# Performance work log

Measured on AMD Instinct MI355X. Metric: run time of the kernel, lower is better.

The kernel has to match this reference:

```python
import jax, jax.numpy as jnp
import numpy as np

H = 128  # hidden size
I = 19   # input size


def _uniform(key, shape, bound):
    return jax.random.uniform(key, shape, dtype=jnp.float32, minval=-bound, maxval=bound)


def setup_inputs() -> dict:
    key = jax.random.key(0)
    ks = jax.random.split(key, 9)
    bound = 1.0 / np.sqrt(H)  # torch nn.RNN init: U(-1/sqrt(H), 1/sqrt(H))
    x = jax.random.normal(ks[0], (256, 1024, I), dtype=jnp.float32)
    return {
        "x": x,
        "W_ih0": _uniform(ks[1], (H, I), bound),
        "W_hh0": _uniform(ks[2], (H, H), bound),
        "b_ih0": _uniform(ks[3], (H,), bound),
        "b_hh0": _uniform(ks[4], (H,), bound),
        "W_ih1": _uniform(ks[5], (H, H), bound),
        "W_hh1": _uniform(ks[6], (H, H), bound),
        "b_ih1": _uniform(ks[7], (H,), bound),
        "b_hh1": _uniform(ks[8], (H,), bound),
    }


def _rnn_layer(inp, W_ih, W_hh, b_ih, b_hh):
    # inp: [B, T, F]. Precompute input projection for all timesteps (one big GEMM),
    # then scan only the recurrent part: h_t = tanh(pre_t + h_{t-1} @ W_hh^T).
    pre = jnp.einsum('btf,hf->bth', inp, W_ih) + b_ih + b_hh  # [B, T, H]
    h0 = jnp.zeros((inp.shape[0], H), dtype=inp.dtype)

    def step(h, p_t):
        h = jnp.tanh(p_t + h @ W_hh.T)
        return h, h

    _, ys = jax.lax.scan(step, h0, jnp.swapaxes(pre, 0, 1))  # ys: [T, B, H]
    return jnp.swapaxes(ys, 0, 1)  # [B, T, H]


def reference(x, W_ih0, W_hh0, b_ih0, b_hh0, W_ih1, W_hh1, b_ih1, b_hh1):
    out1 = _rnn_layer(x, W_ih0, W_hh0, b_ih0, b_hh0)
    out2 = _rnn_layer(out1, W_ih1, W_hh1, b_ih1, b_hh1)
    return out2
```

## Files before the change

kernel.cpp:

```cpp
#include <hip/hip_runtime.h>
#include <math.h>

#define BATCH 256
#define T 1024
#define IN 19
#define H 128

__device__ __forceinline__ float fast_tanh(float x) {
    float ax = fabsf(x);
    float e  = __expf(2.0f * ax);
    float r  = 1.0f - 2.0f / (e + 1.0f);
    return copysignf(r, x);
}

template <int CTRL>
__device__ __forceinline__ float dppf(float v) {
    return __int_as_float(__builtin_amdgcn_update_dpp(
        0, __float_as_int(v), CTRL, 0xF, 0xF, true));
}
#define XOR1 0xB1
#define XOR2 0x4E
#define XOR8 0x128

__device__ __forceinline__ void sync_fast() {
    asm volatile("s_waitcnt lgkmcnt(0)" ::: "memory");
    __builtin_amdgcn_s_barrier();
    asm volatile("" ::: "memory");
}

__device__ __forceinline__ int uoff(int u) { return (u >> 4) * 20 + (u & 15); }

__global__ __launch_bounds__(512, 2)
void fused_rnn(const float* __restrict__ x,
               const float* __restrict__ Wih0,
               const float* __restrict__ Whh0,
               const float* __restrict__ bih0,
               const float* __restrict__ bhh0,
               const float* __restrict__ Wih1,
               const float* __restrict__ Whh1,
               const float* __restrict__ bih1,
               const float* __restrict__ bhh1,
               float* __restrict__ out) {
    const int b   = blockIdx.x;
    const int tid = threadIdx.x;

    __shared__ __align__(16) float h0ring[4][160];
    __shared__ __align__(16) float h1ring[4][160];
    __shared__ __align__(16) float Bring[4][H];
    __shared__ __align__(16) float projring[4][H];
    __shared__ __align__(16) float xbuf[2][8 * 20];

    if (tid < 128) {
        __builtin_amdgcn_s_setprio(1);
        const bool b0 = tid & 1, b1 = tid & 2, b2 = tid & 8;
        const int s    = (tid & 3) | ((tid & 8) >> 1);
        const int G    = (tid >> 4) * 2 + ((tid >> 2) & 1);
        const int ub   = G * 8;
        const int ufin = ub + (b0 ? 4 : 0) + (b1 ? 2 : 0) + (b2 ? 1 : 0);

        float wA[8][16];
#pragma unroll
        for (int u = 0; u < 8; ++u) {
            const float* wr = Whh0 + (size_t)(ub + u) * H + s * 16;
#pragma unroll
            for (int c = 0; c < 16; c += 4) {
                float4 v = *(const float4*)&wr[c];
                wA[u][c] = v.x; wA[u][c+1] = v.y; wA[u][c+2] = v.z; wA[u][c+3] = v.w;
            }
        }
        {
            const float* wr = Wih0 + ufin * IN;
            const float* xr = x + (size_t)b * T * IN;
            float acc = bih0[ufin] + bhh0[ufin];
#pragma unroll
            for (int f = 0; f < IN; ++f) acc = fmaf(xr[f], wr[f], acc);
            projring[0][ufin] = acc;
        }
        h0ring[3][uoff(ufin)] = 0.0f;
        sync_fast();

        const int so = s * 20;
        const int wo = uoff(ufin);
        for (int ko = 0; ko < T; ko += 8) {
#pragma unroll
            for (int j = 0; j < 8; ++j) {
                const float* hp = &h0ring[(j + 3) & 3][so];
                float pcur = projring[j & 3][ufin];
                float d0=0,d1=0,d2=0,d3=0,d4=0,d5=0,d6=0,d7=0;
#pragma unroll
                for (int c = 0; c < 16; c += 4) {
                    float4 hv = *(const float4*)&hp[c];
                    d0 = fmaf(wA[0][c],hv.x,d0); d0 = fmaf(wA[0][c+1],hv.y,d0); d0 = fmaf(wA[0][c+2],hv.z,d0); d0 = fmaf(wA[0][c+3],hv.w,d0);
                    d1 = fmaf(wA[1][c],hv.x,d1); d1 = fmaf(wA[1][c+1],hv.y,d1); d1 = fmaf(wA[1][c+2],hv.z,d1); d1 = fmaf(wA[1][c+3],hv.w,d1);
                    d2 = fmaf(wA[2][c],hv.x,d2); d2 = fmaf(wA[2][c+1],hv.y,d2); d2 = fmaf(wA[2][c+2],hv.z,d2); d2 = fmaf(wA[2][c+3],hv.w,d2);
                    d3 = fmaf(wA[3][c],hv.x,d3); d3 = fmaf(wA[3][c+1],hv.y,d3); d3 = fmaf(wA[3][c+2],hv.z,d3); d3 = fmaf(wA[3][c+3],hv.w,d3);
                    d4 = fmaf(wA[4][c],hv.x,d4); d4 = fmaf(wA[4][c+1],hv.y,d4); d4 = fmaf(wA[4][c+2],hv.z,d4); d4 = fmaf(wA[4][c+3],hv.w,d4);
                    d5 = fmaf(wA[5][c],hv.x,d5); d5 = fmaf(wA[5][c+1],hv.y,d5); d5 = fmaf(wA[5][c+2],hv.z,d5); d5 = fmaf(wA[5][c+3],hv.w,d5);
                    d6 = fmaf(wA[6][c],hv.x,d6); d6 = fmaf(wA[6][c+1],hv.y,d6); d6 = fmaf(wA[6][c+2],hv.z,d6); d6 = fmaf(wA[6][c+3],hv.w,d6);
                    d7 = fmaf(wA[7][c],hv.x,d7); d7 = fmaf(wA[7][c+1],hv.y,d7); d7 = fmaf(wA[7][c+2],hv.z,d7); d7 = fmaf(wA[7][c+3],hv.w,d7);
                }
                float e0 = (b0 ? d4 : d0) + dppf<XOR1>(b0 ? d0 : d4);
                float e1 = (b0 ? d5 : d1) + dppf<XOR1>(b0 ? d1 : d5);
                float e2 = (b0 ? d6 : d2) + dppf<XOR1>(b0 ? d2 : d6);
                float e3 = (b0 ? d7 : d3) + dppf<XOR1>(b0 ? d3 : d7);
                float g0 = (b1 ? e2 : e0) + dppf<XOR2>(b1 ? e0 : e2);
                float g1 = (b1 ? e3 : e1) + dppf<XOR2>(b1 ? e1 : e3);
                float f  = (b2 ? g1 : g0) + dppf<XOR8>(b2 ? g0 : g1);
                h0ring[j & 3][wo] = fast_tanh(pcur + f);
                sync_fast();
            }
        }
        sync_fast();
        sync_fast();
    } else if (tid < 384) {
        const int p  = tid - 128;
        const bool b0 = p & 1, b1 = p & 2;
        const int s    = (p & 3) | ((p & 8) >> 1);
        const int Gp   = (p >> 4) * 2 + ((p >> 2) & 1);
        const int ub   = Gp * 4;
        const int ufin = ub + (b0 ? 2 : 0) + (b1 ? 1 : 0);

        float wP[4][16];
#pragma unroll
        for (int u = 0; u < 4; ++u) {
            const float* wr = Wih1 + (size_t)(ub + u) * H + s * 16;
#pragma unroll
            for (int c = 0; c < 16; c += 4) {
                float4 v = *(const float4*)&wr[c];
                wP[u][c] = v.x; wP[u][c+1] = v.y; wP[u][c+2] = v.z; wP[u][c+3] = v.w;
            }
        }
        const float biasP = bih1[ufin] + bhh1[ufin];

        const bool hasProj = (p >= 128);
        const int pu = p - 128;
        float wIP[20];
        float biasPr = 0.0f;
        const float* xsrc = x + (size_t)b * T * IN + IN;
        const int idx0  = pu;
        const int idx1  = pu + 128;
        const bool v1   = hasProj && (pu < 24);
        const int slot0 = hasProj ? ((idx0 / IN) * 20 + idx0 % IN) : 0;
        const int slot1 = hasProj ? ((idx1 / IN) * 20 + idx1 % IN) : 0;
        const int XMAX  = (T - 1) * IN - 1;
        float xr0 = 0.0f, xr1 = 0.0f;

        if (hasProj) {
            const float* wr = Wih0 + (size_t)pu * IN;
#pragma unroll
            for (int f = 0; f < IN; ++f) wIP[f] = wr[f];
            wIP[19] = 0.0f;
            biasPr = bih0[pu] + bhh0[pu];
            if (pu < 8) { xbuf[0][pu * 20 + 19] = 0.0f; xbuf[1][pu * 20 + 19] = 0.0f; }
            xbuf[0][slot0] = xsrc[idx0];
            if (v1) xbuf[0][slot1] = xsrc[idx1];
            xr0 = xsrc[152 + idx0];
            if (v1) xr1 = xsrc[152 + idx1];
        }
        sync_fast();

        const int so = s * 20;
        for (int ko = 0; ko < T; ko += 8) {
            const int cb = (ko >> 3) & 1;
#pragma unroll
            for (int j = 0; j < 8; ++j) {
                const float* hp = &h0ring[(j + 3) & 3][so];
                float d0=0,d1=0,d2=0,d3=0;
#pragma unroll
                for (int c = 0; c < 16; c += 4) {
                    float4 hv = *(const float4*)&hp[c];
                    d0 = fmaf(wP[0][c],hv.x,d0); d0 = fmaf(wP[0][c+1],hv.y,d0); d0 = fmaf(wP[0][c+2],hv.z,d0); d0 = fmaf(wP[0][c+3],hv.w,d0);
                    d1 = fmaf(wP[1][c],hv.x,d1); d1 = fmaf(wP[1][c+1],hv.y,d1); d1 = fmaf(wP[1][c+2],hv.z,d1); d1 = fmaf(wP[1][c+3],hv.w,d1);
                    d2 = fmaf(wP[2][c],hv.x,d2); d2 = fmaf(wP[2][c+1],hv.y,d2); d2 = fmaf(wP[2][c+2],hv.z,d2); d2 = fmaf(wP[2][c+3],hv.w,d2);
                    d3 = fmaf(wP[3][c],hv.x,d3); d3 = fmaf(wP[3][c+1],hv.y,d3); d3 = fmaf(wP[3][c+2],hv.z,d3); d3 = fmaf(wP[3][c+3],hv.w,d3);
                }
                float e0 = (b0 ? d2 : d0) + dppf<XOR1>(b0 ? d0 : d2);
                float e1 = (b0 ? d3 : d1) + dppf<XOR1>(b0 ? d1 : d3);
                float g  = (b1 ? e1 : e0) + dppf<XOR2>(b1 ? e0 : e1);
                g += dppf<XOR8>(g);
                if (!(p & 8)) Bring[(j + 3) & 3][ufin] = g + biasP;
                if (hasProj) {
                    const float* xp = &xbuf[cb][j * 20];
                    float4 xv0 = *(const float4*)&xp[0];
                    float4 xv1 = *(const float4*)&xp[4];
                    float4 xv2 = *(const float4*)&xp[8];
                    float4 xv3 = *(const float4*)&xp[12];
                    float4 xv4 = *(const float4*)&xp[16];
                    float p0 = biasPr, p1 = 0.0f;
                    p0 = fmaf(xv0.x, wIP[0],  p0); p1 = fmaf(xv0.y, wIP[1],  p1);
                    p0 = fmaf(xv0.z, wIP[2],  p0); p1 = fmaf(xv0.w, wIP[3],  p1);
                    p0 = fmaf(xv1.x, wIP[4],  p0); p1 = fmaf(xv1.y, wIP[5],  p1);
                    p0 = fmaf(xv1.z, wIP[6],  p0); p1 = fmaf(xv1.w, wIP[7],  p1);
                    p0 = fmaf(xv2.x, wIP[8],  p0); p1 = fmaf(xv2.y, wIP[9],  p1);
                    p0 = fmaf(xv2.z, wIP[10], p0); p1 = fmaf(xv2.w, wIP[11], p1);
                    p0 = fmaf(xv3.x, wIP[12], p0); p1 = fmaf(xv3.y, wIP[13], p1);
                    p0 = fmaf(xv3.z, wIP[14], p0); p1 = fmaf(xv3.w, wIP[15], p1);
                    p0 = fmaf(xv4.x, wIP[16], p0); p1 = fmaf(xv4.y, wIP[17], p1);
                    p0 = fmaf(xv4.z, wIP[18], p0); p1 = fmaf(xv4.w, wIP[19], p1);
                    projring[(j + 1) & 3][pu] = p0 + p1;
                    if (j == 7) {
                        float* xd = xbuf[cb ^ 1];
                        xd[slot0] = xr0;
                        if (v1) xd[slot1] = xr1;
                        const int c2 = (ko >> 3) + 2;
                        int o0 = 152 * c2 + idx0; o0 = o0 > XMAX ? XMAX : o0;
                        int o1 = 152 * c2 + idx1; o1 = o1 > XMAX ? XMAX : o1;
                        xr0 = xsrc[o0];
                        if (v1) xr1 = xsrc[o1];
                    }
                }
                sync_fast();
            }
        }
        {
            const float* hp = &h0ring[3][so];
            float d0=0,d1=0,d2=0,d3=0;
#pragma unroll
            for (int c = 0; c < 16; c += 4) {
                float4 hv = *(const float4*)&hp[c];
                d0 = fmaf(wP[0][c],hv.x,d0); d0 = fmaf(wP[0][c+1],hv.y,d0); d0 = fmaf(wP[0][c+2],hv.z,d0); d0 = fmaf(wP[0][c+3],hv.w,d0);
                d1 = fmaf(wP[1][c],hv.x,d1); d1 = fmaf(wP[1][c+1],hv.y,d1); d1 = fmaf(wP[1][c+2],hv.z,d1); d1 = fmaf(wP[1][c+3],hv.w,d1);
                d2 = fmaf(wP[2][c],hv.x,d2); d2 = fmaf(wP[2][c+1],hv.y,d2); d2 = fmaf(wP[2][c+2],hv.z,d2); d2 = fmaf(wP[2][c+3],hv.w,d2);
                d3 = fmaf(wP[3][c],hv.x,d3); d3 = fmaf(wP[3][c+1],hv.y,d3); d3 = fmaf(wP[3][c+2],hv.z,d3); d3 = fmaf(wP[3][c+3],hv.w,d3);
            }
            float e0 = (b0 ? d2 : d0) + dppf<XOR1>(b0 ? d0 : d2);
            float e1 = (b0 ? d3 : d1) + dppf<XOR1>(b0 ? d1 : d3);
            float g  = (b1 ? e1 : e0) + dppf<XOR2>(b1 ? e0 : e1);
            g += dppf<XOR8>(g);
            if (!(p & 8)) Bring[3][ufin] = g + biasP;
        }
        sync_fast();
        sync_fast();
    } else {
        __builtin_amdgcn_s_setprio(1);
        const int w  = tid - 384;
        const bool b0 = w & 1, b1 = w & 2, b2 = w & 8;
        const int s    = (w & 3) | ((w & 8) >> 1);
        const int G    = (w >> 4) * 2 + ((w >> 2) & 1);
        const int ub   = G * 8;
        const int ufin = ub + (b0 ? 4 : 0) + (b1 ? 2 : 0) + (b2 ? 1 : 0);

        float wA[8][16];
#pragma unroll
        for (int u = 0; u < 8; ++u) {
            const float* wr = Whh1 + (size_t)(ub + u) * H + s * 16;
#pragma unroll
            for (int c = 0; c < 16; c += 4) {
                float4 v = *(const float4*)&wr[c];
                wA[u][c] = v.x; wA[u][c+1] = v.y; wA[u][c+2] = v.z; wA[u][c+3] = v.w;
            }
        }
        float* orow = out + (size_t)b * T * H + ufin;
        float sbuf[8];

        h1ring[3][uoff(ufin)] = 0.0f;
        sync_fast();
        sync_fast();
        sync_fast();

        const int so = s * 20;
        const int wo = uoff(ufin);
        for (int ko = 2; ko < 1026; ko += 8) {
#pragma unroll
            for (int j = 0; j < 8; ++j) {
                const float* hp = &h1ring[(j + 3) & 3][so];
                float Bg = Bring[j & 3][ufin];
                float d0=0,d1=0,d2=0,d3=0,d4=0,d5=0,d6=0,d7=0;
#pragma unroll
                for (int c = 0; c < 16; c += 4) {
                    float4 hv = *(const float4*)&hp[c];
                    d0 = fmaf(wA[0][c],hv.x,d0); d0 = fmaf(wA[0][c+1],hv.y,d0); d0 = fmaf(wA[0][c+2],hv.z,d0); d0 = fmaf(wA[0][c+3],hv.w,d0);
                    d1 = fmaf(wA[1][c],hv.x,d1); d1 = fmaf(wA[1][c+1],hv.y,d1); d1 = fmaf(wA[1][c+2],hv.z,d1); d1 = fmaf(wA[1][c+3],hv.w,d1);
                    d2 = fmaf(wA[2][c],hv.x,d2); d2 = fmaf(wA[2][c+1],hv.y,d2); d2 = fmaf(wA[2][c+2],hv.z,d2); d2 = fmaf(wA[2][c+3],hv.w,d2);
                    d3 = fmaf(wA[3][c],hv.x,d3); d3 = fmaf(wA[3][c+1],hv.y,d3); d3 = fmaf(wA[3][c+2],hv.z,d3); d3 = fmaf(wA[3][c+3],hv.w,d3);
                    d4 = fmaf(wA[4][c],hv.x,d4); d4 = fmaf(wA[4][c+1],hv.y,d4); d4 = fmaf(wA[4][c+2],hv.z,d4); d4 = fmaf(wA[4][c+3],hv.w,d4);
                    d5 = fmaf(wA[5][c],hv.x,d5); d5 = fmaf(wA[5][c+1],hv.y,d5); d5 = fmaf(wA[5][c+2],hv.z,d5); d5 = fmaf(wA[5][c+3],hv.w,d5);
                    d6 = fmaf(wA[6][c],hv.x,d6); d6 = fmaf(wA[6][c+1],hv.y,d6); d6 = fmaf(wA[6][c+2],hv.z,d6); d6 = fmaf(wA[6][c+3],hv.w,d6);
                    d7 = fmaf(wA[7][c],hv.x,d7); d7 = fmaf(wA[7][c+1],hv.y,d7); d7 = fmaf(wA[7][c+2],hv.z,d7); d7 = fmaf(wA[7][c+3],hv.w,d7);
                }
                float e0 = (b0 ? d4 : d0) + dppf<XOR1>(b0 ? d0 : d4);
                float e1 = (b0 ? d5 : d1) + dppf<XOR1>(b0 ? d1 : d5);
                float e2 = (b0 ? d6 : d2) + dppf<XOR1>(b0 ? d2 : d6);
                float e3 = (b0 ? d7 : d3) + dppf<XOR1>(b0 ? d3 : d7);
                float g0 = (b1 ? e2 : e0) + dppf<XOR2>(b1 ? e0 : e2);
                float g1 = (b1 ? e3 : e1) + dppf<XOR2>(b1 ? e1 : e3);
                float f  = (b2 ? g1 : g0) + dppf<XOR8>(b2 ? g0 : g1);
                float h1v = fast_tanh(Bg + f);
                h1ring[j & 3][wo] = h1v;
                sbuf[j] = h1v;
                if (j == 7) {
                    const int t0 = ko - 2;
#pragma unroll
                    for (int i = 0; i < 8; ++i)
                        orow[(size_t)(t0 + i) * H] = sbuf[i];
                }
                sync_fast();
            }
        }
    }
}

extern "C" void kernel_launch(void* const* d_in, const int* in_sizes, int n_in,
                              void* d_out, int out_size, void* d_ws, size_t ws_size,
                              hipStream_t stream) {
    const float* x     = (const float*)d_in[0];
    const float* W_ih0 = (const float*)d_in[1];
    const float* W_hh0 = (const float*)d_in[2];
    const float* b_ih0 = (const float*)d_in[3];
    const float* b_hh0 = (const float*)d_in[4];
    const float* W_ih1 = (const float*)d_in[5];
    const float* W_hh1 = (const float*)d_in[6];
    const float* b_ih1 = (const float*)d_in[7];
    const float* b_hh1 = (const float*)d_in[8];

    float* out = (float*)d_out;

    fused_rnn<<<BATCH, 512, 0, stream>>>(x, W_ih0, W_hh0, b_ih0, b_hh0,
                                         W_ih1, W_hh1, b_ih1, b_hh1, out);
}
```

Baseline: 608.7 us.

## Deepen middle-stage pipeline so layer-1 input projection lags one extra step

The middle warp group, which computes W_ih1·h0 for layer 1, now loads h0 into alternating register buffers and computes from the buffer loaded in the previous step. This decouples the shared-memory load from the FMA chain inside each barrier interval. The pipeline gains one more stage: every role adds an extra barrier, and the layer-1 recurrence loop shifts by one step. The aim is to hide LDS latency on the critical path of each step, at the cost of one extra step of pipeline fill and more registers.

```diff
diff --git a/kernel.cpp b/kernel.cpp
--- a/kernel.cpp
+++ b/kernel.cpp
@@ -112,6 +112,7 @@
         }
         sync_fast();
         sync_fast();
+        sync_fast();
     } else if (tid < 384) {
         const int p  = tid - 128;
         const bool b0 = p & 1, b1 = p & 2;
@@ -157,30 +158,75 @@
             xr0 = xsrc[152 + idx0];
             if (v1) xr1 = xsrc[152 + idx1];
         }
-        sync_fast();
+
+        float4 z4 = {0.0f, 0.0f, 0.0f, 0.0f};
+        float4 hA0 = z4, hA1 = z4, hA2 = z4, hA3 = z4;
+        float4 hB0 = z4, hB1 = z4, hB2 = z4, hB3 = z4;
+
+        sync_fast();
+
+#define P_BCOMP(c0, c1, c2v, c3v, BSLOT)                                              \
+        {                                                                             \
+            float d0=0,d1=0,d2=0,d3=0;                                                \
+            d0 = fmaf(wP[0][0],  c0.x, d0); d0 = fmaf(wP[0][1],  c0.y, d0);           \
+            d0 = fmaf(wP[0][2],  c0.z, d0); d0 = fmaf(wP[0][3],  c0.w, d0);           \
+            d1 = fmaf(wP[1][0],  c0.x, d1); d1 = fmaf(wP[1][1],  c0.y, d1);           \
+            d1 = fmaf(wP[1][2],  c0.z, d1); d1 = fmaf(wP[1][3],  c0.w, d1);           \
+            d2 = fmaf(wP[2][0],  c0.x, d2); d2 = fmaf(wP[2][1],  c0.y, d2);           \
+            d2 = fmaf(wP[2][2],  c0.z, d2); d2 = fmaf(wP[2][3],  c0.w, d2);           \
+            d3 = fmaf(wP[3][0],  c0.x, d3); d3 = fmaf(wP[3][1],  c0.y, d3);           \
+            d3 = fmaf(wP[3][2],  c0.z, d3); d3 = fmaf(wP[3][3],  c0.w, d3);           \
+            d0 = fmaf(wP[0][4],  c1.x, d0); d0 = fmaf(wP[0][5],  c1.y, d0);           \
+            d0 = fmaf(wP[0][6],  c1.z, d0); d0 = fmaf(wP[0][7],  c1.w, d0);           \
+            d1 = fmaf(wP[1][4],  c1.x, d1); d1 = fmaf(wP[1][5],  c1.y, d1);           \
+            d1 = fmaf(wP[1][6],  c1.z, d1); d1 = fmaf(wP[1][7],  c1.w, d1);           \
+            d2 = fmaf(wP[2][4],  c1.x, d2); d2 = fmaf(wP[2][5],  c1.y, d2);           \
+            d2 = fmaf(wP[2][6],  c1.z, d2); d2 = fmaf(wP[2][7],  c1.w, d2);           \
+            d3 = fmaf(wP[3][4],  c1.x, d3); d3 = fmaf(wP[3][5],  c1.y, d3);           \
+            d3 = fmaf(wP[3][6],  c1.z, d3); d3 = fmaf(wP[3][7],  c1.w, d3);           \
+            d0 = fmaf(wP[0][8],  c2v.x, d0); d0 = fmaf(wP[0][9],  c2v.y, d0);         \
+            d0 = fmaf(wP[0][10], c2v.z, d0); d0 = fmaf(wP[0][11], c2v.w, d0);         \
+            d1 = fmaf(wP[1][8],  c2v.x, d1); d1 = fmaf(wP[1][9],  c2v.y, d1);         \
+            d1 = fmaf(wP[1][10], c2v.z, d1); d1 = fmaf(wP[1][11], c2v.w, d1);         \
+            d2 = fmaf(wP[2][8],  c2v.x, d2); d2 = fmaf(wP[2][9],  c2v.y, d2);         \
+            d2 = fmaf(wP[2][10], c2v.z, d2); d2 = fmaf(wP[2][11], c2v.w, d2);         \
+            d3 = fmaf(wP[3][8],  c2v.x, d3); d3 = fmaf(wP[3][9],  c2v.y, d3);         \
+            d3 = fmaf(wP[3][10], c2v.z, d3); d3 = fmaf(wP[3][11], c2v.w, d3);         \
+            d0 = fmaf(wP[0][12], c3v.x, d0); d0 = fmaf(wP[0][13], c3v.y, d0);         \
+            d0 = fmaf(wP[0][14], c3v.z, d0); d0 = fmaf(wP[0][15], c3v.w, d0);         \
+            d1 = fmaf(wP[1][12], c3v.x, d1); d1 = fmaf(wP[1][13], c3v.y, d1);         \
+            d1 = fmaf(wP[1][14], c3v.z, d1); d1 = fmaf(wP[1][15], c3v.w, d1);         \
+            d2 = fmaf(wP[2][12], c3v.x, d2); d2 = fmaf(wP[2][13], c3v.y, d2);         \
+            d2 = fmaf(wP[2][14], c3v.z, d2); d2 = fmaf(wP[2][15], c3v.w, d2);         \
+            d3 = fmaf(wP[3][12], c3v.x, d3); d3 = fmaf(wP[3][13], c3v.y, d3);         \
+            d3 = fmaf(wP[3][14], c3v.z, d3); d3 = fmaf(wP[3][15], c3v.w, d3);         \
+            float e0 = (b0 ? d2 : d0) + dppf<XOR1>(b0 ? d0 : d2);                     \
+            float e1 = (b0 ? d3 : d1) + dppf<XOR1>(b0 ? d1 : d3);                     \
+            float g  = (b1 ? e1 : e0) + dppf<XOR2>(b1 ? e0 : e1);                     \
+            g += dppf<XOR8>(g);                                                       \
+            if (!(p & 8)) Bring[BSLOT][ufin] = g + biasP;                             \
+        }
 
         const int so = s * 20;
         for (int ko = 0; ko < T; ko += 8) {
             const int cb = (ko >> 3) & 1;
 #pragma unroll
-            for (int j = 0; j < 8; ++j) {
-                const float* hp = &h0ring[(j + 3) & 3][so];
-                float d0=0,d1=0,d2=0,d3=0;
-#pragma unroll
-                for (int c = 0; c < 16; c += 4) {
-                    float4 hv = *(const float4*)&hp[c];
-                    d0 = fmaf(wP[0][c],hv.x,d0); d0 = fmaf(wP[0][c+1],hv.y,d0); d0 = fmaf(wP[0][c+2],hv.z,d0); d0 = fmaf(wP[0][c+3],hv.w,d0);
-                    d1 = fmaf(wP[1][c],hv.x,d1); d1 = fmaf(wP[1][c+1],hv.y,d1); d1 = fmaf(wP[1][c+2],hv.z,d1); d1 = fmaf(wP[1][c+3],hv.w,d1);
-                    d2 = fmaf(wP[2][c],hv.x,d2); d2 = fmaf(wP[2][c+1],hv.y,d2); d2 = fmaf(wP[2][c+2],hv.z,d2); d2 = fmaf(wP[2][c+3],hv.w,d2);
-                    d3 = fmaf(wP[3][c],hv.x,d3); d3 = fmaf(wP[3][c+1],hv.y,d3); d3 = fmaf(wP[3][c+2],hv.z,d3); d3 = fmaf(wP[3][c+3],hv.w,d3);
-                }
-                float e0 = (b0 ? d2 : d0) + dppf<XOR1>(b0 ? d0 : d2);
-                float e1 = (b0 ? d3 : d1) + dppf<XOR1>(b0 ? d1 : d3);
-                float g  = (b1 ? e1 : e0) + dppf<XOR2>(b1 ? e0 : e1);
-                g += dppf<XOR8>(g);
-                if (!(p & 8)) Bring[(j + 3) & 3][ufin] = g + biasP;
+            for (int jj = 0; jj < 8; ++jj) {
+                const float* hp = &h0ring[(jj + 3) & 3][so];
+                if ((jj & 1) == 0) {
+                    hA0 = *(const float4*)&hp[0];  hA1 = *(const float4*)&hp[4];
+                    hA2 = *(const float4*)&hp[8];  hA3 = *(const float4*)&hp[12];
+                } else {
+                    hB0 = *(const float4*)&hp[0];  hB1 = *(const float4*)&hp[4];
+                    hB2 = *(const float4*)&hp[8];  hB3 = *(const float4*)&hp[12];
+                }
+                if ((jj & 1) == 0) {
+                    P_BCOMP(hB0, hB1, hB2, hB3, ((jj + 2) & 3))
+                } else {
+                    P_BCOMP(hA0, hA1, hA2, hA3, ((jj + 2) & 3))
+                }
                 if (hasProj) {
-                    const float* xp = &xbuf[cb][j * 20];
+                    const float* xp = &xbuf[cb][jj * 20];
                     float4 xv0 = *(const float4*)&xp[0];
                     float4 xv1 = *(const float4*)&xp[4];
                     float4 xv2 = *(const float4*)&xp[8];
@@ -197,8 +243,8 @@
                     p0 = fmaf(xv3.z, wIP[14], p0); p1 = fmaf(xv3.w, wIP[15], p1);
                     p0 = fmaf(xv4.x, wIP[16], p0); p1 = fmaf(xv4.y, wIP[17], p1);
                     p0 = fmaf(xv4.z, wIP[18], p0); p1 = fmaf(xv4.w, wIP[19], p1);
-                    projring[(j + 1) & 3][pu] = p0 + p1;
-                    if (j == 7) {
+                    projring[(jj + 1) & 3][pu] = p0 + p1;
+                    if (jj == 7) {
                         float* xd = xbuf[cb ^ 1];
                         xd[slot0] = xr0;
                         if (v1) xd[slot1] = xr1;
@@ -214,23 +260,15 @@
         }
         {
             const float* hp = &h0ring[3][so];
-            float d0=0,d1=0,d2=0,d3=0;
-#pragma unroll
-            for (int c = 0; c < 16; c += 4) {
-                float4 hv = *(const float4*)&hp[c];
-                d0 = fmaf(wP[0][c],hv.x,d0); d0 = fmaf(wP[0][c+1],hv.y,d0); d0 = fmaf(wP[0][c+2],hv.z,d0); d0 = fmaf(wP[0][c+3],hv.w,d0);
-                d1 = fmaf(wP[1][c],hv.x,d1); d1 = fmaf(wP[1][c+1],hv.y,d1); d1 = fmaf(wP[1][c+2],hv.z,d1); d1 = fmaf(wP[1][c+3],hv.w,d1);
-                d2 = fmaf(wP[2][c],hv.x,d2); d2 = fmaf(wP[2][c+1],hv.y,d2); d2 = fmaf(wP[2][c+2],hv.z,d2); d2 = fmaf(wP[2][c+3],hv.w,d2);
-                d3 = fmaf(wP[3][c],hv.x,d3); d3 = fmaf(wP[3][c+1],hv.y,d3); d3 = fmaf(wP[3][c+2],hv.z,d3); d3 = fmaf(wP[3][c+3],hv.w,d3);
-            }
-            float e0 = (b0 ? d2 : d0) + dppf<XOR1>(b0 ? d0 : d2);
-            float e1 = (b0 ? d3 : d1) + dppf<XOR1>(b0 ? d1 : d3);
-            float g  = (b1 ? e1 : e0) + dppf<XOR2>(b1 ? e0 : e1);
-            g += dppf<XOR8>(g);
-            if (!(p & 8)) Bring[3][ufin] = g + biasP;
-        }
-        sync_fast();
-        sync_fast();
+            hA0 = *(const float4*)&hp[0];  hA1 = *(const float4*)&hp[4];
+            hA2 = *(const float4*)&hp[8];  hA3 = *(const float4*)&hp[12];
+            P_BCOMP(hB0, hB1, hB2, hB3, 2)
+        }
+        sync_fast();
+        P_BCOMP(hA0, hA1, hA2, hA3, 3)
+        sync_fast();
+        sync_fast();
+#undef P_BCOMP
     } else {
         __builtin_amdgcn_s_setprio(1);
         const int w  = tid - 384;
@@ -257,10 +295,11 @@
         sync_fast();
         sync_fast();
         sync_fast();
+        sync_fast();
 
         const int so = s * 20;
         const int wo = uoff(ufin);
-        for (int ko = 2; ko < 1026; ko += 8) {
+        for (int ko = 3; ko < 1027; ko += 8) {
 #pragma unroll
             for (int j = 0; j < 8; ++j) {
                 const float* hp = &h1ring[(j + 3) & 3][so];
@@ -289,7 +328,7 @@
                 h1ring[j & 3][wo] = h1v;
                 sbuf[j] = h1v;
                 if (j == 7) {
-                    const int t0 = ko - 2;
+                    const int t0 = ko - 3;
 #pragma unroll
                     for (int i = 0; i < 8; ++i)
                         orow[(size_t)(t0 + i) * H] = sbuf[i];
```

Result: slower. 664.9 us (+9.2%).
